# Kernel optimization log

Hardware: AMD Instinct MI355X
Metric: run time of the kernel (lower is better)

Reference implementation:

```python
import jax, jax.numpy as jnp
import numpy as np

TEMPERATURE = 0.5


def setup_inputs() -> dict:
    key = jax.random.key(0)
    k1, k2 = jax.random.split(key)
    B, C, H, W = 64, 256, 32, 32
    inputs = jax.random.normal(k1, (B, C, H, W), dtype=jnp.float32)
    targets = jax.random.normal(k2, (B, C, H, W), dtype=jnp.float32)
    return {"inputs": inputs, "targets": targets}


def reference(inputs, targets):
    # [B, C, H, W] -> [H, W, B, C]
    x = jnp.transpose(inputs, (2, 3, 0, 1))
    y = jnp.transpose(targets, (2, 3, 0, 1))
    B = x.shape[-2]
    feats = jnp.concatenate([x, y], axis=-2)  # [H, W, 2B, C]
    eps = jnp.finfo(feats.dtype).eps
    # cosine similarity: normalize each vector with eps-clamped norm, then dot
    norms = jnp.maximum(jnp.linalg.norm(feats, axis=-1, keepdims=True), eps)
    fn = feats / norms
    sim = jnp.einsum('hwic,hwjc->hwij', fn, fn)  # [H, W, 2B, 2B]
    # mask self-similarity diagonal with -inf
    mask = jnp.eye(2 * B, dtype=bool)
    sim = jnp.where(mask, -jnp.inf, sim)
    log_sm = jax.nn.log_softmax(sim / TEMPERATURE, axis=-1)
    pos = jnp.concatenate(
        [jnp.diagonal(log_sm, offset=B, axis1=-2, axis2=-1),
         jnp.diagonal(log_sm, offset=-B, axis1=-2, axis2=-1)],
        axis=-1,
    )  # [H, W, 2B]
    return -jnp.mean(pos)
```

## Files before the change

### kernel.cpp

```cpp
#include <hip/hip_runtime.h>
#include <stdint.h>

#define HWPOS 1024
#define CCH   256
#define RROWS 128
#define EPSF  1.1920928955078125e-07f

typedef __attribute__((ext_vector_type(4))) float float4v;

__device__ float g_acc[64 * 16];

__device__ __forceinline__ uint32_t pk4_fp8(float a, float b, float c, float d) {
  int v = 0;
  v = __builtin_amdgcn_cvt_pk_fp8_f32(a, b, v, false);
  v = __builtin_amdgcn_cvt_pk_fp8_f32(c, d, v, true);
  return (uint32_t)v;
}


__global__ __launch_bounds__(512, 2) void k_transpose(const float* __restrict__ inp,
                                                      const float* __restrict__ tgt,
                                                      unsigned char* __restrict__ wsF) {
  __shared__ float T[16 * 1024];
  const int t = threadIdx.x;
  const int r = blockIdx.x;
  const int q = blockIdx.y;
  if (r == 0 && q == 0 && t < 64) g_acc[t * 16] = 0.0f;
  const float* src = (r < 64) ? (inp + (size_t)r * CCH * HWPOS)
                              : (tgt + (size_t)(r - 64) * CCH * HWPOS);
  const int c_l = t >> 5;
  const int l32 = t & 31;
  const int qs  = q ^ ((r >> 2) & 3);
  const size_t regbase = (size_t)(r * 4 + qs) * 65536;
#pragma unroll
  for (int k = 0; k < 4; ++k) {
    const int dd = q * 4 + k;
    const float* gp = src + (size_t)(dd * 16 + c_l) * HWPOS + l32 * 4;
    float4 v[8];
#pragma unroll
    for (int j = 0; j < 8; ++j) v[j] = *(const float4*)(gp + j * 128);
#pragma unroll
    for (int j = 0; j < 8; ++j)
      *(float4*)&T[c_l * 1024 + l32 * 4 + j * 128] = v[j];
    __syncthreads();
    const int sl3 = k ^ (r & 3);
#pragma unroll
    for (int h2 = 0; h2 < 2; ++h2) {
      const int hw = t + h2 * 512;
      float x[16];
#pragma unroll
      for (int c = 0; c < 16; ++c) x[c] = T[c * 1024 + hw];
      uint4 o;
      o.x = pk4_fp8(x[0],  x[1],  x[2],  x[3]);
      o.y = pk4_fp8(x[4],  x[5],  x[6],  x[7]);
      o.z = pk4_fp8(x[8],  x[9],  x[10], x[11]);
      o.w = pk4_fp8(x[12], x[13], x[14], x[15]);
      *(uint4*)(wsF + regbase + (size_t)hw * 64 + sl3 * 16) = o;
    }
    __syncthreads();
  }
}

__global__ __launch_bounds__(512, 4) void k_gram(const unsigned char* __restrict__ wsF) {
  __shared__ unsigned char Fs[32768];
  __shared__ float sInv[RROWS];
  __shared__ float wred[8];
  const int t  = threadIdx.x;
  const int hw = blockIdx.x;
  const int lane = t & 63;
  const int w    = t >> 6;
  const int lid  = lane & 15;
  const int quad = lane >> 4;
  float4v acc[8];
#pragma unroll
  for (int ni = 0; ni < 8; ++ni) acc[ni] = (float4v){0.f, 0.f, 0.f, 0.f};
#pragma unroll
  for (int it = 0; it < 4; ++it) {
    const int ch = it * 512 + t;
    const int rr = ch >> 4;
    const int ss = ch & 15;
    const size_t goff = (size_t)((rr << 2) + (ss >> 2)) * 65536
                      + (size_t)hw * 64 + (size_t)(ss & 3) * 16;
    __builtin_amdgcn_global_load_lds(
        (const __attribute__((address_space(1))) unsigned int*)(wsF + goff),
        (__attribute__((address_space(3))) unsigned int*)(Fs + (size_t)ch * 16),
        16, 0, 0);
  }
  __syncthreads();
  const int rowA = (w << 4) | lid;
#pragma unroll
  for (int ks = 0; ks < 8; ++ks) {
    const int d    = 2 * ks + (quad >> 1);
    const int off  = ((d ^ lid) << 4) + (quad & 1) * 8;
    long a = *(const long*)&Fs[rowA * 256 + off];
#pragma unroll
    for (int ni = 0; ni < 8; ++ni) {
      long b = *(const long*)&Fs[(((ni << 4) | lid)) * 256 + off];
      acc[ni] = __builtin_amdgcn_mfma_f32_16x16x32_fp8_fp8(a, b, acc[ni], 0, 0, 0);
    }
  }
  {
    float diagv = 0.f;
#pragma unroll
    for (int ni = 0; ni < 8; ++ni) {
      if (ni == w) {
#pragma unroll
        for (int e = 0; e < 4; ++e)
          if (e == (lid & 3)) diagv = acc[ni][e];
      }
    }
    if ((lid >> 2) == quad) {
      sInv[(w << 4) | lid] = 1.0f / fmaxf(sqrtf(diagv), EPSF);
    }
  }
  __syncthreads();
  float invj[8];
#pragma unroll
  for (int ni = 0; ni < 8; ++ni) invj[ni] = sInv[(ni << 4) | lid];
  const int tj = (w + 4) & 7;
  float lacc = 0.f;
#pragma unroll
  for (int reg = 0; reg < 4; ++reg) {
    const int rloc = quad * 4 + reg;
    const int rg   = (w << 4) | rloc;
    const float invi = sInv[rg];
    float v[8];
#pragma unroll
    for (int ni = 0; ni < 8; ++ni) v[ni] = 2.0f * acc[ni][reg] * invi * invj[ni];
#pragma unroll
    for (int ni = 0; ni < 8; ++ni)
      if (ni == w && lid == rloc) v[ni] = -3.0e38f;
    float mx = v[0];
#pragma unroll
    for (int ni = 1; ni < 8; ++ni) mx = fmaxf(mx, v[ni]);
#pragma unroll
    for (int sh = 1; sh < 16; sh <<= 1) mx = fmaxf(mx, __shfl_xor(mx, sh, 16));
    float sm = 0.f;
#pragma unroll
    for (int ni = 0; ni < 8; ++ni) sm += __expf(v[ni] - mx);
#pragma unroll
    for (int sh = 1; sh < 16; sh <<= 1) sm += __shfl_xor(sm, sh, 16);
    const float lse = mx + __logf(sm);
    float cand = 0.f;
#pragma unroll
    for (int ni = 0; ni < 8; ++ni)
      if (ni == tj) cand = v[ni];
    const float vp = __shfl(cand, rloc, 16);
    lacc += vp - lse;
  }
#pragma unroll
  for (int sh = 1; sh < 64; sh <<= 1) lacc += __shfl_xor(lacc, sh, 64);
  if (lane == 0) wred[w] = lacc;
  __syncthreads();
  if (t == 0) {
    float tot = 0.f;
#pragma unroll
    for (int i = 0; i < 8; ++i) tot += wred[i];
    atomicAdd(&g_acc[(hw & 63) * 16], tot);
  }
}

__global__ __launch_bounds__(64) void k_reduce(float* __restrict__ out) {
  const int t = threadIdx.x;
  float v = g_acc[t * 16];
#pragma unroll
  for (int sh = 1; sh < 64; sh <<= 1) v += __shfl_xor(v, sh, 64);
  if (t == 0) out[0] = -v * (1.0f / 2097152.0f);
}

extern "C" void kernel_launch(void* const* d_in, const int* in_sizes, int n_in,
                              void* d_out, int out_size, void* d_ws, size_t ws_size,
                              hipStream_t stream) {
  const float* inp = (const float*)d_in[0];
  const float* tgt = (const float*)d_in[1];
  unsigned char* wsF = (unsigned char*)d_ws;
  k_transpose<<<dim3(128, 4), 512, 0, stream>>>(inp, tgt, wsF);
  k_gram<<<dim3(HWPOS), 512, 0, stream>>>(wsF);
  k_reduce<<<1, 64, 0, stream>>>((float*)d_out);
}
```

Baseline: 178.4 us.

## Restructure transpose into smaller blocks with direct-to-LDS loads and row-contiguous fp8 layout

The transpose kernel now runs 1024 smaller 256-thread blocks, splitting the spatial range in half. Each block fills LDS straight from global memory with global_load_lds instead of staging through registers. It packs four 16-channel fp8 chunks in registers and writes 64 contiguous bytes per position into a new workspace layout of [row][hw][256 channels]. The gram kernel's load addressing changes to match this layout and keeps the same XOR swizzle, so each hw row is one contiguous 256-byte read. The aims are more parallelism, wider coalesced stores in the transpose, and more contiguous loads in the gram kernel, at the cost of extra registers to hold the packed chunks.

```diff
diff --git a/kernel.cpp b/kernel.cpp
--- a/kernel.cpp
+++ b/kernel.cpp
@@ -18,46 +18,62 @@
 }
 
 
-__global__ __launch_bounds__(512, 2) void k_transpose(const float* __restrict__ inp,
+__global__ __launch_bounds__(256, 4) void k_transpose(const float* __restrict__ inp,
                                                       const float* __restrict__ tgt,
                                                       unsigned char* __restrict__ wsF) {
-  __shared__ float T[16 * 1024];
-  const int t = threadIdx.x;
-  const int r = blockIdx.x;
-  const int q = blockIdx.y;
-  if (r == 0 && q == 0 && t < 64) g_acc[t * 16] = 0.0f;
+  __shared__ float T[16 * 512];
+  const int t    = threadIdx.x;
+  const int r    = blockIdx.x;
+  const int cq   = blockIdx.y;
+  const int hwh  = blockIdx.z;
+  if (r == 0 && cq == 0 && hwh == 0 && t < 64) g_acc[t * 16] = 0.0f;
   const float* src = (r < 64) ? (inp + (size_t)r * CCH * HWPOS)
                               : (tgt + (size_t)(r - 64) * CCH * HWPOS);
-  const int c_l = t >> 5;
-  const int l32 = t & 31;
-  const int qs  = q ^ ((r >> 2) & 3);
-  const size_t regbase = (size_t)(r * 4 + qs) * 65536;
+  const int lane = t & 63;
+  const int wv   = t >> 6;
+  uint4 a0[4], a1[4];
 #pragma unroll
-  for (int k = 0; k < 4; ++k) {
-    const int dd = q * 4 + k;
-    const float* gp = src + (size_t)(dd * 16 + c_l) * HWPOS + l32 * 4;
-    float4 v[8];
+  for (int dl = 0; dl < 4; ++dl) {
+    const int c0 = cq * 64 + dl * 16;
 #pragma unroll
-    for (int j = 0; j < 8; ++j) v[j] = *(const float4*)(gp + j * 128);
-#pragma unroll
-    for (int j = 0; j < 8; ++j)
-      *(float4*)&T[c_l * 1024 + l32 * 4 + j * 128] = v[j];
-    __syncthreads();
-    const int sl3 = k ^ (r & 3);
-#pragma unroll
-    for (int h2 = 0; h2 < 2; ++h2) {
-      const int hw = t + h2 * 512;
-      float x[16];
-#pragma unroll
-      for (int c = 0; c < 16; ++c) x[c] = T[c * 1024 + hw];
-      uint4 o;
-      o.x = pk4_fp8(x[0],  x[1],  x[2],  x[3]);
-      o.y = pk4_fp8(x[4],  x[5],  x[6],  x[7]);
-      o.z = pk4_fp8(x[8],  x[9],  x[10], x[11]);
-      o.w = pk4_fp8(x[12], x[13], x[14], x[15]);
-      *(uint4*)(wsF + regbase + (size_t)hw * 64 + sl3 * 16) = o;
+    for (int j = 0; j < 8; ++j) {
+      const int row = wv * 4 + (j >> 1);
+      const int seg = j & 1;
+      const float* gp = src + (size_t)(c0 + row) * HWPOS
+                      + hwh * 512 + seg * 256 + lane * 4;
+      __builtin_amdgcn_global_load_lds(
+          (const __attribute__((address_space(1))) unsigned int*)gp,
+          (__attribute__((address_space(3))) unsigned int*)
+              ((unsigned char*)T + row * 2048 + seg * 1024 + lane * 16),
+          16, 0, 0);
     }
     __syncthreads();
+    float x0[16], x1[16];
+#pragma unroll
+    for (int c = 0; c < 16; ++c) { x0[c] = T[c * 512 + t];
+                                   x1[c] = T[c * 512 + t + 256]; }
+    uint4 o0, o1;
+    o0.x = pk4_fp8(x0[0],  x0[1],  x0[2],  x0[3]);
+    o0.y = pk4_fp8(x0[4],  x0[5],  x0[6],  x0[7]);
+    o0.z = pk4_fp8(x0[8],  x0[9],  x0[10], x0[11]);
+    o0.w = pk4_fp8(x0[12], x0[13], x0[14], x0[15]);
+    o1.x = pk4_fp8(x1[0],  x1[1],  x1[2],  x1[3]);
+    o1.y = pk4_fp8(x1[4],  x1[5],  x1[6],  x1[7]);
+    o1.z = pk4_fp8(x1[8],  x1[9],  x1[10], x1[11]);
+    o1.w = pk4_fp8(x1[12], x1[13], x1[14], x1[15]);
+#pragma unroll
+    for (int d2 = 0; d2 < 4; ++d2) {
+      if (d2 == dl) { a0[d2] = o0; a1[d2] = o1; }
+    }
+    if (dl < 3) __syncthreads();
+  }
+  unsigned char* w0 = wsF + (size_t)r * 262144
+                    + (size_t)(hwh * 512 + t) * 256 + cq * 64;
+  unsigned char* w1 = w0 + (size_t)256 * 256;
+#pragma unroll
+  for (int dl = 0; dl < 4; ++dl) {
+    *(uint4*)(w0 + dl * 16) = a0[dl];
+    *(uint4*)(w1 + dl * 16) = a1[dl];
   }
 }
 
@@ -79,8 +95,9 @@
     const int ch = it * 512 + t;
     const int rr = ch >> 4;
     const int ss = ch & 15;
-    const size_t goff = (size_t)((rr << 2) + (ss >> 2)) * 65536
-                      + (size_t)hw * 64 + (size_t)(ss & 3) * 16;
+    const int dd = ss ^ (rr & 15);
+    const size_t goff = (size_t)rr * 262144 + (size_t)hw * 256
+                      + (size_t)dd * 16;
     __builtin_amdgcn_global_load_lds(
         (const __attribute__((address_space(1))) unsigned int*)(wsF + goff),
         (__attribute__((address_space(3))) unsigned int*)(Fs + (size_t)ch * 16),
@@ -174,7 +191,7 @@
   const float* inp = (const float*)d_in[0];
   const float* tgt = (const float*)d_in[1];
   unsigned char* wsF = (unsigned char*)d_ws;
-  k_transpose<<<dim3(128, 4), 512, 0, stream>>>(inp, tgt, wsF);
+  k_transpose<<<dim3(128, 4, 2), 256, 0, stream>>>(inp, tgt, wsF);
   k_gram<<<dim3(HWPOS), 512, 0, stream>>>(wsF);
   k_reduce<<<1, 64, 0, stream>>>((float*)d_out);
 }
```

Result: faster. 173.2 us (-2.9%).
